# Kernel optimization log

Measured on AMD Instinct MI355X. Metric: run time of the kernel, lower is better.

## Reference

```python
import jax, jax.numpy as jnp
import numpy as np

EPS = 1e-5  # torch LayerNorm default

def _std(x):
    # standardize over the last 3 (tensor-feature) modes, biased variance like torch LayerNorm
    mu = jnp.mean(x, axis=(-3, -2, -1), keepdims=True)
    var = jnp.mean(jnp.square(x - mu), axis=(-3, -2, -1), keepdims=True)
    return (x - mu) * jax.lax.rsqrt(var + EPS)

def setup_inputs() -> dict:
    key = jax.random.key(0)
    ks = jax.random.split(key, 12)
    T, B = 512, 16
    a = b = c = 16          # input tensor modes (4096 features)
    ha = hb = hc = 8        # hidden tensor modes (512 features)
    G = 3                   # gates: r, z, n
    f32 = jnp.float32
    return {
        "x": jax.random.normal(ks[0], (T, B, a, b, c), f32),
        "h0": jnp.zeros((B, ha, hb, hc), f32),
        # input-to-hidden TCL3D factors + rank-1 bias + LN affines (stacked over 3 gates)
        "W_fa": jax.random.normal(ks[1], (G, a, ha), f32),
        "W_fb": jax.random.normal(ks[2], (G, b, hb), f32),
        "W_fc": jax.random.normal(ks[3], (G, c, hc), f32),
        "W_ba": jax.random.normal(ks[4], (G, ha), f32),
        "W_bb": jax.random.normal(ks[5], (G, hb), f32),
        "W_bc": jax.random.normal(ks[6], (G, hc), f32),
        "W_lnin_w": jnp.ones((G, a, b, c), f32),
        "W_lnin_b": jnp.zeros((G, a, b, c), f32),
        "W_lnout_w": jnp.ones((G, ha, hb, hc), f32),
        "W_lnout_b": jnp.zeros((G, ha, hb, hc), f32),
        # hidden-to-hidden TCL3D factors + rank-1 bias + LN affines
        "U_fa": jax.random.normal(ks[7], (G, ha, ha), f32),
        "U_fb": jax.random.normal(ks[8], (G, hb, hb), f32),
        "U_fc": jax.random.normal(ks[9], (G, hc, hc), f32),
        "U_ba": jax.random.normal(ks[10], (G, ha), f32),
        "U_bb": jax.random.normal(ks[11], (G, hb), f32),
        "U_bc": jax.random.normal(jax.random.fold_in(key, 99), (G, hc), f32),
        "U_lnin_w": jnp.ones((G, ha, hb, hc), f32),
        "U_lnin_b": jnp.zeros((G, ha, hb, hc), f32),
        "U_lnout_w": jnp.ones((G, ha, hb, hc), f32),
        "U_lnout_b": jnp.zeros((G, ha, hb, hc), f32),
    }

def reference(x, h0, W_fa, W_fb, W_fc, W_ba, W_bb, W_bc,
              W_lnin_w, W_lnin_b, W_lnout_w, W_lnout_b,
              U_fa, U_fb, U_fc, U_ba, U_bb, U_bc,
              U_lnin_w, U_lnin_b, U_lnout_w, U_lnout_b):
    # --- input-to-hidden TCL3D for all 3 gates, batched over time (no h dependence) ---
    xh = _std(x)                                                  # [T,B,a,b,c]
    xg = xh[None] * W_lnin_w[:, None, None] + W_lnin_b[:, None, None]  # [3,T,B,a,b,c]
    Wx = jnp.einsum('gtnabc,gad,gbe,gcf->gtndef', xg, W_fa, W_fb, W_fc)
    Wx = Wx + (W_ba[:, None, None, :, None, None]
               * W_bb[:, None, None, None, :, None]
               * W_bc[:, None, None, None, None, :])              # rank-1 bias
    Wx = _std(Wx) * W_lnout_w[:, None, None] + W_lnout_b[:, None, None]
    Wx = jnp.swapaxes(Wx, 0, 1)                                   # [T,3,B,ha,hb,hc]

    Ub = (U_ba[:, None, :, None, None]
          * U_bb[:, None, None, :, None]
          * U_bc[:, None, None, None, :])                         # [3,1,ha,hb,hc]

    def step(h, wx):
        # hidden-to-hidden TCL3D for all 3 gates
        hh = _std(h)                                              # [B,ha,hb,hc]
        hg = hh[None] * U_lnin_w[:, None] + U_lnin_b[:, None]     # [3,B,ha,hb,hc]
        Uh = jnp.einsum('gndef,gdp,geq,gfr->gnpqr', hg, U_fa, U_fb, U_fc) + Ub
        Uh = _std(Uh) * U_lnout_w[:, None] + U_lnout_b[:, None]
        r = jax.nn.sigmoid(wx[0] + Uh[0])
        z = jax.nn.sigmoid(wx[1] + Uh[1])
        n = jnp.tanh(wx[2] + r * Uh[2])
        h_new = (1.0 - z) * n + z * h
        return h_new, h_new

    _, outs = jax.lax.scan(step, h0, Wx)                          # [T,B,ha,hb,hc]
    return outs
```

## Files before the change

### kernel.cpp

```cpp
#include <hip/hip_runtime.h>

#define EPSV 1e-5f

#define KEEPV(x) asm volatile("" : "+v"(x))
#define KEEPS(x) asm volatile("" : "+s"(x))

#define DPP_XADD(v, ctrl)                                                  \
    v += __int_as_float(__builtin_amdgcn_update_dpp(                       \
        0, __float_as_int(v), ctrl, 0xF, 0xF, false))

__device__ __forceinline__ float wave_allsum(float v) {
    DPP_XADD(v, 0x128);
    DPP_XADD(v, 0x124);
    DPP_XADD(v, 0x122);
    DPP_XADD(v, 0x121);
    DPP_XADD(v, 0x142);
    DPP_XADD(v, 0x143);
    return __int_as_float(__builtin_amdgcn_readlane(__float_as_int(v), 63));
}

__device__ __forceinline__ void bar_lds() {
    asm volatile("s_waitcnt lgkmcnt(0)\n\ts_barrier" ::: "memory");
}

__global__ __launch_bounds__(256) void wx_kernel(
    const float* __restrict__ x,
    const float* __restrict__ Wfa, const float* __restrict__ Wfb,
    const float* __restrict__ Wfc,
    const float* __restrict__ Wba, const float* __restrict__ Wbb,
    const float* __restrict__ Wbc,
    const float* __restrict__ lniw, const float* __restrict__ lnib,
    const float* __restrict__ lnow, const float* __restrict__ lnob,
    float* __restrict__ wxo)
{
    __shared__ float POOL[4096 + 3*2048];
    __shared__ float baS[24], bbS[24], bcS[24];
    __shared__ float red[48];

    float* Xs = POOL;
    float* S1 = POOL + 4096;
    float* S2 = POOL;

    const int tid  = threadIdx.x;
    const int wid  = tid >> 6, lane = tid & 63;
    const size_t tb = blockIdx.x;
    const float* xp = x + tb * 4096;

    float s = 0.f, s2 = 0.f;
    for (int i = tid; i < 1024; i += 256) {
        const float4 v4 = ((const float4*)xp)[i];
        ((float4*)Xs)[i] = v4;
        s  += v4.x + v4.y + v4.z + v4.w;
        s2 += v4.x*v4.x + v4.y*v4.y + v4.z*v4.z + v4.w*v4.w;
    }
    if (tid < 24) { baS[tid] = Wba[tid]; bbS[tid] = Wbb[tid]; bcS[tid] = Wbc[tid]; }

    #pragma unroll
    for (int off = 32; off > 0; off >>= 1) {
        s  += __shfl_down(s,  off);
        s2 += __shfl_down(s2, off);
    }
    if (lane == 0) { red[wid] = s; red[8 + wid] = s2; }
    __syncthreads();
    s  = red[0] + red[1] + red[2] + red[3];
    s2 = red[8] + red[9] + red[10] + red[11];
    const float muX = s * (1.f / 4096.f);
    const float rsX = rsqrtf(fmaxf(s2 * (1.f / 4096.f) - muX * muX, 0.f) + EPSV);

    const int qh = __builtin_amdgcn_readfirstlane(tid >> 7);
    const int rh = __builtin_amdgcn_readfirstlane(tid >> 6);

    {
        float acc[3][8];
        #pragma unroll
        for (int g = 0; g < 3; ++g)
            #pragma unroll
            for (int p = 0; p < 8; ++p) acc[g][p] = 0.f;
        const int rest = tid;
        #pragma unroll
        for (int m = 0; m < 16; ++m) {
            const float xn = (Xs[m*256 + rest] - muX) * rsX;
            #pragma unroll
            for (int g = 0; g < 3; ++g) {
                const float xv = fmaf(xn, lniw[g*4096 + m*256 + rest],
                                      lnib[g*4096 + m*256 + rest]);
                #pragma unroll
                for (int p = 0; p < 8; ++p)
                    acc[g][p] = fmaf(xv, Wfa[(g*16 + m)*8 + p], acc[g][p]);
            }
        }
        #pragma unroll
        for (int g = 0; g < 3; ++g)
            #pragma unroll
            for (int p = 0; p < 8; ++p)
                S1[g*2048 + p*256 + (rest ^ (p << 3))] = acc[g][p];
    }
    __syncthreads();

    {
        float acc[3][4];
        #pragma unroll
        for (int g = 0; g < 3; ++g)
            #pragma unroll
            for (int j = 0; j < 4; ++j) acc[g][j] = 0.f;
        const int rest2 = tid & 127;
        const int c2 = rest2 >> 3, p2 = rest2 & 7;
        #pragma unroll
        for (int m = 0; m < 16; ++m) {
            const int off1 = p2*256 + (((m << 4) | c2) ^ (p2 << 3));
            #pragma unroll
            for (int g = 0; g < 3; ++g) {
                const float xv = S1[g*2048 + off1];
                #pragma unroll
                for (int j = 0; j < 4; ++j)
                    acc[g][j] = fmaf(xv, Wfb[(g*16 + m)*8 + qh*4 + j], acc[g][j]);
            }
        }
        #pragma unroll
        for (int g = 0; g < 3; ++g)
            #pragma unroll
            for (int j = 0; j < 4; ++j) {
                const int q = qh*4 + j;
                S2[g*1024 + q*128 + (rest2 ^ (q << 3))] = acc[g][j];
            }
    }
    __syncthreads();

    float v0[3], v1[3]; int idx0;
    {
        const int rest3 = tid & 63;
        const int q3 = rest3 & 7, pp = rest3 >> 3;
        float acc[3][2];
        #pragma unroll
        for (int g = 0; g < 3; ++g) { acc[g][0] = 0.f; acc[g][1] = 0.f; }
        #pragma unroll
        for (int m = 0; m < 16; ++m) {
            const int off2 = q3*128 + (((m << 3) | pp) ^ (q3 << 3));
            #pragma unroll
            for (int g = 0; g < 3; ++g) {
                const float xv = S2[g*1024 + off2];
                #pragma unroll
                for (int j = 0; j < 2; ++j)
                    acc[g][j] = fmaf(xv, Wfc[(g*16 + m)*8 + rh*2 + j], acc[g][j]);
            }
        }
        #pragma unroll
        for (int g = 0; g < 3; ++g) {
            const float bpq = baS[g*8 + pp] * bbS[g*8 + q3];
            v0[g] = acc[g][0] + bpq * bcS[g*8 + rh*2 + 0];
            v1[g] = acc[g][1] + bpq * bcS[g*8 + rh*2 + 1];
        }
        idx0 = rest3 * 8 + rh * 2;
    }

    {
        float t[3], t2[3];
        #pragma unroll
        for (int g = 0; g < 3; ++g) {
            t[g]  = v0[g] + v1[g];
            t2[g] = v0[g]*v0[g] + v1[g]*v1[g];
        }
        #pragma unroll
        for (int off = 32; off > 0; off >>= 1)
            #pragma unroll
            for (int g = 0; g < 3; ++g) {
                t[g]  += __shfl_down(t[g],  off);
                t2[g] += __shfl_down(t2[g], off);
            }
        if (lane == 0)
            #pragma unroll
            for (int g = 0; g < 3; ++g) {
                red[(g*2 + 0)*8 + wid] = t[g];
                red[(g*2 + 1)*8 + wid] = t2[g];
            }
        __syncthreads();
        #pragma unroll
        for (int g = 0; g < 3; ++g) {
            const float ts  = red[(g*2+0)*8+0] + red[(g*2+0)*8+1]
                            + red[(g*2+0)*8+2] + red[(g*2+0)*8+3];
            const float t2s = red[(g*2+1)*8+0] + red[(g*2+1)*8+1]
                            + red[(g*2+1)*8+2] + red[(g*2+1)*8+3];
            const float mu  = ts * (1.f / 512.f);
            const float var = fmaxf(t2s * (1.f / 512.f) - mu * mu, 0.f);
            const float rs  = rsqrtf(var + EPSV);
            float* wp = wxo + (tb * 3 + g) * 512;
            const float2 lw2 = *(const float2*)(lnow + g*512 + idx0);
            const float2 lb2 = *(const float2*)(lnob + g*512 + idx0);
            float2 o2;
            o2.x = fmaf((v0[g] - mu) * rs, lw2.x, lb2.x);
            o2.y = fmaf((v1[g] - mu) * rs, lw2.y, lb2.y);
            *(float2*)(wp + idx0) = o2;
        }
    }
}

__global__ __launch_bounds__(192)
__attribute__((amdgpu_waves_per_eu(1, 1)))
void scan_kernel(
    const float* __restrict__ wx,
    const float* __restrict__ h0,
    const float* __restrict__ Ufa, const float* __restrict__ Ufb,
    const float* __restrict__ Ufc,
    const float* __restrict__ Uba, const float* __restrict__ Ubb,
    const float* __restrict__ Ubc,
    const float* __restrict__ lniw, const float* __restrict__ lnib,
    const float* __restrict__ lnow, const float* __restrict__ lnob,
    float* __restrict__ out,
    int T, int B)
{
    const int n    = blockIdx.x;
    const int tid  = threadIdx.x;
    const int lane = tid & 63;
    const int gu   = __builtin_amdgcn_readfirstlane(tid >> 6);

    __shared__ float hgS[3][576];
    __shared__ float T1S[3][576];
    __shared__ float T2S[3][576];
    __shared__ float UhS[2][3][576];

    float wA[64], wB[64], wC[64];
    #pragma unroll
    for (int i = 0; i < 64; ++i) {
        wA[i] = __uint_as_float(__builtin_amdgcn_readfirstlane(
                    __float_as_uint(Ufa[gu*64 + i])));
        KEEPS(wA[i]);
    }
    #pragma unroll
    for (int i = 0; i < 64; ++i) { wB[i] = Ufb[gu*64 + i]; KEEPV(wB[i]); }
    #pragma unroll
    for (int i = 0; i < 64; ++i) { wC[i] = Ufc[gu*64 + i]; KEEPV(wC[i]); }

    float lnwT[8], lnbT[8], low8[8], lob8[8], ubias[8];
    {
        const int p_ = lane >> 3, q_ = lane & 7;
        const float bpq = Uba[gu*8 + p_] * Ubb[gu*8 + q_];
        #pragma unroll
        for (int k = 0; k < 8; ++k) {
            lnwT[k]  = lniw[gu*512 + k*64 + lane];
            lnbT[k]  = lnib[gu*512 + k*64 + lane];
            low8[k]  = lnow[gu*512 + lane*8 + k];
            lob8[k]  = lnob[gu*512 + lane*8 + k];
            ubias[k] = bpq * Ubc[gu*8 + k];
        }
    }

    const int wbase = lane;
    const int rbase = (lane & 7) * 72 + (lane >> 3);

    float hv[8];
    {
        const float4 a = *(const float4*)(h0 + n*512 + lane*8);
        const float4 b = *(const float4*)(h0 + n*512 + lane*8 + 4);
        hv[0]=a.x; hv[1]=a.y; hv[2]=a.z; hv[3]=a.w;
        hv[4]=b.x; hv[5]=b.y; hv[6]=b.z; hv[7]=b.w;
    }

    float uo[8];
    float pf[3][8];

#define LOADWX(TT)                                                         \
    {                                                                      \
        const float* base_ = wx + (((size_t)(TT) * B + n) * 3) * 512       \
                             + lane * 8;                                   \
        _Pragma("unroll")                                                  \
        for (int gg = 0; gg < 3; ++gg) {                                   \
            const float4 A_ = *(const float4*)(base_ + gg*512);            \
            const float4 B_ = *(const float4*)(base_ + gg*512 + 4);        \
            pf[gg][0]=A_.x; pf[gg][1]=A_.y; pf[gg][2]=A_.z; pf[gg][3]=A_.w;\
            pf[gg][4]=B_.x; pf[gg][5]=B_.y; pf[gg][6]=B_.z; pf[gg][7]=B_.w;\
        }                                                                  \
    }

#define WR8(BUFROW, V)                                                     \
    {                                                                      \
        float* p0_ = (BUFROW) + wbase;                                     \
        float* p1_ = p0_ + 288;                                            \
        p0_[0] = V[0]; p0_[72] = V[1]; p0_[144] = V[2]; p0_[216] = V[3];   \
        p1_[0] = V[4]; p1_[72] = V[5]; p1_[144] = V[6]; p1_[216] = V[7];   \
    }

#define RD8(BUFROW, V)                                                     \
    {                                                                      \
        const float* q_ = (BUFROW) + rbase;                                \
        V[0] = q_[0];  V[1] = q_[8];  V[2] = q_[16]; V[3] = q_[24];        \
        V[4] = q_[32]; V[5] = q_[40]; V[6] = q_[48]; V[7] = q_[56];        \
    }

#define RD8W(BUFROW, V)                                                    \
    {                                                                      \
        const float* q0_ = (BUFROW) + wbase;                               \
        const float* q1_ = q0_ + 288;                                      \
        V[0] = q0_[0]; V[1] = q0_[72]; V[2] = q0_[144]; V[3] = q0_[216];   \
        V[4] = q1_[0]; V[5] = q1_[72]; V[6] = q1_[144]; V[7] = q1_[216];   \
    }

#define PIPELINE(PARN)                                                     \
    {                                                                      \
        float xv_[8];                                                      \
        RD8(hgS[gu], xv_)                                                  \
        float sA = 0.f, sB = 0.f;                                          \
        _Pragma("unroll")                                                  \
        for (int k = 0; k < 8; ++k) { sA += hv[k]; sB += hv[k]*hv[k]; }    \
        sA = wave_allsum(sA); sB = wave_allsum(sB);                        \
        const float mu_ = sA * (1.f/512.f);                                \
        const float rs_ = rsqrtf(fmaxf(sB*(1.f/512.f) - mu_*mu_, 0.f)      \
                                 + EPSV);                                  \
        float a_[8];                                                       \
        _Pragma("unroll") for (int k = 0; k < 8; ++k) a_[k] = 0.f;         \
        _Pragma("unroll")                                                  \
        for (int m = 0; m < 8; ++m) {                                      \
            const float hgv = fmaf((xv_[m]-mu_)*rs_, lnwT[m], lnbT[m]);    \
            _Pragma("unroll")                                              \
            for (int q = 0; q < 8; ++q)                                    \
                a_[q] = fmaf(hgv, wA[m*8 + q], a_[q]);                     \
        }                                                                  \
        WR8(T1S[gu], a_)                                                   \
        RD8(T1S[gu], xv_)                                                  \
        _Pragma("unroll") for (int k = 0; k < 8; ++k) a_[k] = 0.f;         \
        _Pragma("unroll")                                                  \
        for (int m = 0; m < 8; ++m) {                                      \
            _Pragma("unroll")                                              \
            for (int q = 0; q < 8; ++q)                                    \
                a_[q] = fmaf(xv_[m], wB[m*8 + q], a_[q]);                  \
        }                                                                  \
        WR8(T2S[gu], a_)                                                   \
        RD8(T2S[gu], xv_)                                                  \
        _Pragma("unroll") for (int k = 0; k < 8; ++k) a_[k] = 0.f;         \
        _Pragma("unroll")                                                  \
        for (int m = 0; m < 8; ++m) {                                      \
            _Pragma("unroll")                                              \
            for (int q = 0; q < 8; ++q)                                    \
                a_[q] = fmaf(xv_[m], wC[m*8 + q], a_[q]);                  \
        }                                                                  \
        float sC = 0.f, sD = 0.f;                                          \
        _Pragma("unroll")                                                  \
        for (int k = 0; k < 8; ++k) {                                      \
            a_[k] += ubias[k]; sC += a_[k]; sD += a_[k]*a_[k];             \
        }                                                                  \
        sC = wave_allsum(sC); sD = wave_allsum(sD);                        \
        const float mu2_ = sC * (1.f/512.f);                               \
        const float rs2_ = rsqrtf(fmaxf(sD*(1.f/512.f) - mu2_*mu2_, 0.f)   \
                                  + EPSV);                                 \
        _Pragma("unroll")                                                  \
        for (int k = 0; k < 8; ++k)                                        \
            uo[k] = fmaf((a_[k]-mu2_)*rs2_, low8[k], lob8[k]);             \
        WR8(UhS[PARN][gu], uo)                                             \
    }

#define COMBINE(PARC, TT)                                                  \
    {                                                                      \
        float ur[8], uz[8], un[8];                                         \
        if (gu == 0) {                                                     \
            _Pragma("unroll")                                              \
            for (int k = 0; k < 8; ++k) ur[k] = uo[k];                     \
            RD8W(UhS[PARC][1], uz)                                         \
            RD8W(UhS[PARC][2], un)                                         \
        } else if (gu == 1) {                                              \
            _Pragma("unroll")                                              \
            for (int k = 0; k < 8; ++k) uz[k] = uo[k];                     \
            RD8W(UhS[PARC][0], ur)                                         \
            RD8W(UhS[PARC][2], un)                                         \
        } else {                                                           \
            _Pragma("unroll")                                              \
            for (int k = 0; k < 8; ++k) un[k] = uo[k];                     \
            RD8W(UhS[PARC][0], ur)                                         \
            RD8W(UhS[PARC][1], uz)                                         \
        }                                                                  \
        _Pragma("unroll")                                                  \
        for (int k = 0; k < 8; ++k) {                                      \
            const float er_ = __expf(-(pf[0][k] + ur[k]));                 \
            const float r_  = __builtin_amdgcn_rcpf(1.f + er_);            \
            const float ez_ = __expf(-(pf[1][k] + uz[k]));                 \
            const float z_  = __builtin_amdgcn_rcpf(1.f + ez_);            \
            const float e2_ = __expf(2.f * (pf[2][k] + r_ * un[k]));       \
            const float nn_ = 1.f - 2.f*__builtin_amdgcn_rcpf(e2_ + 1.f);  \
            hv[k] = (1.f - z_)*nn_ + z_*hv[k];                             \
        }                                                                  \
        WR8(hgS[gu], hv)      \
        if (gu == 0) {                                                     \
            float* op_ = out + ((size_t)(TT) * B + n) * 512 + lane*8;      \
            *(float4*)op_     = make_float4(hv[0], hv[1], hv[2], hv[3]);   \
            *(float4*)(op_+4) = make_float4(hv[4], hv[5], hv[6], hv[7]);   \
        }                                                                  \
    }

    LOADWX(0);
    WR8(hgS[gu], hv)
    PIPELINE(0);

    for (int t = 0; t < T; t += 2) {
        bar_lds();
        COMBINE(0, t)
        if (t + 1 < T) {
            LOADWX(t + 1);
            PIPELINE(1)
        }
        bar_lds();
        if (t + 1 < T) COMBINE(1, t + 1)
        if (t + 2 < T) {
            LOADWX(t + 2);
            PIPELINE(0)
        }
    }
#undef LOADWX
#undef WR8
#undef RD8
#undef RD8W
#undef PIPELINE
#undef COMBINE
}

extern "C" void kernel_launch(void* const* d_in, const int* in_sizes, int n_in,
                              void* d_out, int out_size, void* d_ws, size_t ws_size,
                              hipStream_t stream)
{
    const float* x    = (const float*)d_in[0];
    const float* h0   = (const float*)d_in[1];
    const float* Wfa  = (const float*)d_in[2];
    const float* Wfb  = (const float*)d_in[3];
    const float* Wfc  = (const float*)d_in[4];
    const float* Wba  = (const float*)d_in[5];
    const float* Wbb  = (const float*)d_in[6];
    const float* Wbc  = (const float*)d_in[7];
    const float* Wliw = (const float*)d_in[8];
    const float* Wlib = (const float*)d_in[9];
    const float* Wlow = (const float*)d_in[10];
    const float* Wlob = (const float*)d_in[11];
    const float* Ufa  = (const float*)d_in[12];
    const float* Ufb  = (const float*)d_in[13];
    const float* Ufc  = (const float*)d_in[14];
    const float* Uba  = (const float*)d_in[15];
    const float* Ubb  = (const float*)d_in[16];
    const float* Ubc  = (const float*)d_in[17];
    const float* Uliw = (const float*)d_in[18];
    const float* Ulib = (const float*)d_in[19];
    const float* Ulow = (const float*)d_in[20];
    const float* Ulob = (const float*)d_in[21];

    const int B = in_sizes[1] / 512;
    const int T = in_sizes[0] / (B * 4096);

    float* wxws = (float*)d_ws;
    float* out  = (float*)d_out;

    wx_kernel<<<T * B, 256, 0, stream>>>(x, Wfa, Wfb, Wfc, Wba, Wbb, Wbc,
                                         Wliw, Wlib, Wlow, Wlob, wxws);
    scan_kernel<<<B, 192, 0, stream>>>(wxws, h0, Ufa, Ufb, Ufc, Uba, Ubb, Ubc,
                                       Uliw, Ulib, Ulow, Ulob, out, T, B);
}
```

Before: 797.7 us.

## Fuse input projection and recurrent scan into one persistent kernel with chunk flags

Merges the per-timestep input TCL kernel and the sequential scan kernel into one launch. B blocks run the recurrence while 240 worker blocks compute Wx chunks of 16 timesteps and signal completion through global atomic counters, which the scan blocks poll before loading each chunk. The aim is to overlap the parallel input projection with the latency-bound scan instead of running them back to back. The scan blocks now launch with 256 threads and an idle fourth wave that only matches barriers. The design relies on all blocks being co-resident to avoid deadlock. The fallback branch passes a fixed shift that may not match other shapes.

```diff
diff --git a/kernel.cpp b/kernel.cpp
--- a/kernel.cpp
+++ b/kernel.cpp
@@ -4,6 +4,8 @@
 
 #define KEEPV(x) asm volatile("" : "+v"(x))
 #define KEEPS(x) asm volatile("" : "+s"(x))
+
+__device__ unsigned g_cnt[64];
 
 #define DPP_XADD(v, ctrl)                                                  \
     v += __int_as_float(__builtin_amdgcn_update_dpp(                       \
@@ -23,200 +25,219 @@
     asm volatile("s_waitcnt lgkmcnt(0)\n\ts_barrier" ::: "memory");
 }
 
-__global__ __launch_bounds__(256) void wx_kernel(
+__global__ void init_flags() {
+    if (threadIdx.x < 64) g_cnt[threadIdx.x] = 0u;
+}
+
+__global__ __launch_bounds__(256)
+__attribute__((amdgpu_waves_per_eu(1, 1)))
+void fused_kernel(
     const float* __restrict__ x,
     const float* __restrict__ Wfa, const float* __restrict__ Wfb,
     const float* __restrict__ Wfc,
     const float* __restrict__ Wba, const float* __restrict__ Wbb,
     const float* __restrict__ Wbc,
-    const float* __restrict__ lniw, const float* __restrict__ lnib,
-    const float* __restrict__ lnow, const float* __restrict__ lnob,
-    float* __restrict__ wxo)
-{
-    __shared__ float POOL[4096 + 3*2048];
-    __shared__ float baS[24], bbS[24], bcS[24];
-    __shared__ float red[48];
-
-    float* Xs = POOL;
-    float* S1 = POOL + 4096;
-    float* S2 = POOL;
-
-    const int tid  = threadIdx.x;
-    const int wid  = tid >> 6, lane = tid & 63;
-    const size_t tb = blockIdx.x;
-    const float* xp = x + tb * 4096;
-
-    float s = 0.f, s2 = 0.f;
-    for (int i = tid; i < 1024; i += 256) {
-        const float4 v4 = ((const float4*)xp)[i];
-        ((float4*)Xs)[i] = v4;
-        s  += v4.x + v4.y + v4.z + v4.w;
-        s2 += v4.x*v4.x + v4.y*v4.y + v4.z*v4.z + v4.w*v4.w;
-    }
-    if (tid < 24) { baS[tid] = Wba[tid]; bbS[tid] = Wbb[tid]; bcS[tid] = Wbc[tid]; }
-
-    #pragma unroll
-    for (int off = 32; off > 0; off >>= 1) {
-        s  += __shfl_down(s,  off);
-        s2 += __shfl_down(s2, off);
-    }
-    if (lane == 0) { red[wid] = s; red[8 + wid] = s2; }
-    __syncthreads();
-    s  = red[0] + red[1] + red[2] + red[3];
-    s2 = red[8] + red[9] + red[10] + red[11];
-    const float muX = s * (1.f / 4096.f);
-    const float rsX = rsqrtf(fmaxf(s2 * (1.f / 4096.f) - muX * muX, 0.f) + EPSV);
-
-    const int qh = __builtin_amdgcn_readfirstlane(tid >> 7);
-    const int rh = __builtin_amdgcn_readfirstlane(tid >> 6);
-
-    {
-        float acc[3][8];
-        #pragma unroll
-        for (int g = 0; g < 3; ++g)
-            #pragma unroll
-            for (int p = 0; p < 8; ++p) acc[g][p] = 0.f;
-        const int rest = tid;
-        #pragma unroll
-        for (int m = 0; m < 16; ++m) {
-            const float xn = (Xs[m*256 + rest] - muX) * rsX;
-            #pragma unroll
-            for (int g = 0; g < 3; ++g) {
-                const float xv = fmaf(xn, lniw[g*4096 + m*256 + rest],
-                                      lnib[g*4096 + m*256 + rest]);
-                #pragma unroll
-                for (int p = 0; p < 8; ++p)
-                    acc[g][p] = fmaf(xv, Wfa[(g*16 + m)*8 + p], acc[g][p]);
-            }
-        }
-        #pragma unroll
-        for (int g = 0; g < 3; ++g)
-            #pragma unroll
-            for (int p = 0; p < 8; ++p)
-                S1[g*2048 + p*256 + (rest ^ (p << 3))] = acc[g][p];
-    }
-    __syncthreads();
-
-    {
-        float acc[3][4];
-        #pragma unroll
-        for (int g = 0; g < 3; ++g)
-            #pragma unroll
-            for (int j = 0; j < 4; ++j) acc[g][j] = 0.f;
-        const int rest2 = tid & 127;
-        const int c2 = rest2 >> 3, p2 = rest2 & 7;
-        #pragma unroll
-        for (int m = 0; m < 16; ++m) {
-            const int off1 = p2*256 + (((m << 4) | c2) ^ (p2 << 3));
-            #pragma unroll
-            for (int g = 0; g < 3; ++g) {
-                const float xv = S1[g*2048 + off1];
-                #pragma unroll
-                for (int j = 0; j < 4; ++j)
-                    acc[g][j] = fmaf(xv, Wfb[(g*16 + m)*8 + qh*4 + j], acc[g][j]);
-            }
-        }
-        #pragma unroll
-        for (int g = 0; g < 3; ++g)
-            #pragma unroll
-            for (int j = 0; j < 4; ++j) {
-                const int q = qh*4 + j;
-                S2[g*1024 + q*128 + (rest2 ^ (q << 3))] = acc[g][j];
-            }
-    }
-    __syncthreads();
-
-    float v0[3], v1[3]; int idx0;
-    {
-        const int rest3 = tid & 63;
-        const int q3 = rest3 & 7, pp = rest3 >> 3;
-        float acc[3][2];
-        #pragma unroll
-        for (int g = 0; g < 3; ++g) { acc[g][0] = 0.f; acc[g][1] = 0.f; }
-        #pragma unroll
-        for (int m = 0; m < 16; ++m) {
-            const int off2 = q3*128 + (((m << 3) | pp) ^ (q3 << 3));
-            #pragma unroll
-            for (int g = 0; g < 3; ++g) {
-                const float xv = S2[g*1024 + off2];
-                #pragma unroll
-                for (int j = 0; j < 2; ++j)
-                    acc[g][j] = fmaf(xv, Wfc[(g*16 + m)*8 + rh*2 + j], acc[g][j]);
-            }
-        }
-        #pragma unroll
-        for (int g = 0; g < 3; ++g) {
-            const float bpq = baS[g*8 + pp] * bbS[g*8 + q3];
-            v0[g] = acc[g][0] + bpq * bcS[g*8 + rh*2 + 0];
-            v1[g] = acc[g][1] + bpq * bcS[g*8 + rh*2 + 1];
-        }
-        idx0 = rest3 * 8 + rh * 2;
-    }
-
-    {
-        float t[3], t2[3];
-        #pragma unroll
-        for (int g = 0; g < 3; ++g) {
-            t[g]  = v0[g] + v1[g];
-            t2[g] = v0[g]*v0[g] + v1[g]*v1[g];
-        }
-        #pragma unroll
-        for (int off = 32; off > 0; off >>= 1)
-            #pragma unroll
-            for (int g = 0; g < 3; ++g) {
-                t[g]  += __shfl_down(t[g],  off);
-                t2[g] += __shfl_down(t2[g], off);
-            }
-        if (lane == 0)
-            #pragma unroll
-            for (int g = 0; g < 3; ++g) {
-                red[(g*2 + 0)*8 + wid] = t[g];
-                red[(g*2 + 1)*8 + wid] = t2[g];
-            }
-        __syncthreads();
-        #pragma unroll
-        for (int g = 0; g < 3; ++g) {
-            const float ts  = red[(g*2+0)*8+0] + red[(g*2+0)*8+1]
-                            + red[(g*2+0)*8+2] + red[(g*2+0)*8+3];
-            const float t2s = red[(g*2+1)*8+0] + red[(g*2+1)*8+1]
-                            + red[(g*2+1)*8+2] + red[(g*2+1)*8+3];
-            const float mu  = ts * (1.f / 512.f);
-            const float var = fmaxf(t2s * (1.f / 512.f) - mu * mu, 0.f);
-            const float rs  = rsqrtf(var + EPSV);
-            float* wp = wxo + (tb * 3 + g) * 512;
-            const float2 lw2 = *(const float2*)(lnow + g*512 + idx0);
-            const float2 lb2 = *(const float2*)(lnob + g*512 + idx0);
-            float2 o2;
-            o2.x = fmaf((v0[g] - mu) * rs, lw2.x, lb2.x);
-            o2.y = fmaf((v1[g] - mu) * rs, lw2.y, lb2.y);
-            *(float2*)(wp + idx0) = o2;
-        }
-    }
-}
-
-__global__ __launch_bounds__(192)
-__attribute__((amdgpu_waves_per_eu(1, 1)))
-void scan_kernel(
-    const float* __restrict__ wx,
+    const float* __restrict__ Wliw, const float* __restrict__ Wlib,
+    const float* __restrict__ Wlow, const float* __restrict__ Wlob,
+    float* __restrict__ wxo,
     const float* __restrict__ h0,
     const float* __restrict__ Ufa, const float* __restrict__ Ufb,
     const float* __restrict__ Ufc,
     const float* __restrict__ Uba, const float* __restrict__ Ubb,
     const float* __restrict__ Ubc,
-    const float* __restrict__ lniw, const float* __restrict__ lnib,
-    const float* __restrict__ lnow, const float* __restrict__ lnob,
-    float* __restrict__ out,
-    int T, int B)
+    const float* __restrict__ Uliw, const float* __restrict__ Ulib,
+    const float* __restrict__ Ulow, const float* __restrict__ Ulob,
+    float* __restrict__ out, int T, int B, int nWx, int cshift)
 {
-    const int n    = blockIdx.x;
+    __shared__ __align__(16) float smem[10368];
     const int tid  = threadIdx.x;
     const int lane = tid & 63;
-    const int gu   = __builtin_amdgcn_readfirstlane(tid >> 6);
-
-    __shared__ float hgS[3][576];
-    __shared__ float T1S[3][576];
-    __shared__ float T2S[3][576];
-    __shared__ float UhS[2][3][576];
+
+    if ((int)blockIdx.x >= B) {
+        const int w  = blockIdx.x - B;
+        const int TB = T * B;
+        float* Xs  = smem;
+        float* S1  = smem + 4096;
+        float* S2  = smem;
+        float* baS = smem + 10240;
+        float* bbS = smem + 10264;
+        float* bcS = smem + 10288;
+        float* red = smem + 10312;
+
+        if (tid < 24) { baS[tid] = Wba[tid]; bbS[tid] = Wbb[tid]; bcS[tid] = Wbc[tid]; }
+        const int wid = tid >> 6;
+        const int qh = __builtin_amdgcn_readfirstlane(tid >> 7);
+        const int rh = __builtin_amdgcn_readfirstlane(tid >> 6);
+
+        for (int tb = w; tb < TB; tb += nWx) {
+            const float* xp = x + (size_t)tb * 4096;
+            float s = 0.f, s2 = 0.f;
+            for (int i = tid; i < 1024; i += 256) {
+                const float4 v4 = ((const float4*)xp)[i];
+                ((float4*)Xs)[i] = v4;
+                s  += v4.x + v4.y + v4.z + v4.w;
+                s2 += v4.x*v4.x + v4.y*v4.y + v4.z*v4.z + v4.w*v4.w;
+            }
+            #pragma unroll
+            for (int off = 32; off > 0; off >>= 1) {
+                s  += __shfl_down(s,  off);
+                s2 += __shfl_down(s2, off);
+            }
+            if (lane == 0) { red[wid] = s; red[8 + wid] = s2; }
+            __syncthreads();
+            s  = red[0] + red[1] + red[2] + red[3];
+            s2 = red[8] + red[9] + red[10] + red[11];
+            const float muX = s * (1.f / 4096.f);
+            const float rsX = rsqrtf(fmaxf(s2 * (1.f / 4096.f) - muX*muX, 0.f) + EPSV);
+
+            {
+                float acc[3][8];
+                #pragma unroll
+                for (int g = 0; g < 3; ++g)
+                    #pragma unroll
+                    for (int p = 0; p < 8; ++p) acc[g][p] = 0.f;
+                const int rest = tid;
+                #pragma unroll
+                for (int m = 0; m < 16; ++m) {
+                    const float xn = (Xs[m*256 + rest] - muX) * rsX;
+                    #pragma unroll
+                    for (int g = 0; g < 3; ++g) {
+                        const float xv = fmaf(xn, Wliw[g*4096 + m*256 + rest],
+                                              Wlib[g*4096 + m*256 + rest]);
+                        #pragma unroll
+                        for (int p = 0; p < 8; ++p)
+                            acc[g][p] = fmaf(xv, Wfa[(g*16 + m)*8 + p], acc[g][p]);
+                    }
+                }
+                #pragma unroll
+                for (int g = 0; g < 3; ++g)
+                    #pragma unroll
+                    for (int p = 0; p < 8; ++p)
+                        S1[g*2048 + p*256 + (rest ^ (p << 3))] = acc[g][p];
+            }
+            __syncthreads();
+
+            {
+                float acc[3][4];
+                #pragma unroll
+                for (int g = 0; g < 3; ++g)
+                    #pragma unroll
+                    for (int j = 0; j < 4; ++j) acc[g][j] = 0.f;
+                const int rest2 = tid & 127;
+                const int c2 = rest2 >> 3, p2 = rest2 & 7;
+                #pragma unroll
+                for (int m = 0; m < 16; ++m) {
+                    const int off1 = p2*256 + (((m << 4) | c2) ^ (p2 << 3));
+                    #pragma unroll
+                    for (int g = 0; g < 3; ++g) {
+                        const float xv = S1[g*2048 + off1];
+                        #pragma unroll
+                        for (int j = 0; j < 4; ++j)
+                            acc[g][j] = fmaf(xv, Wfb[(g*16 + m)*8 + qh*4 + j], acc[g][j]);
+                    }
+                }
+                #pragma unroll
+                for (int g = 0; g < 3; ++g)
+                    #pragma unroll
+                    for (int j = 0; j < 4; ++j) {
+                        const int q = qh*4 + j;
+                        S2[g*1024 + q*128 + (rest2 ^ (q << 3))] = acc[g][j];
+                    }
+            }
+            __syncthreads();
+
+            float v0[3], v1[3]; int idx0;
+            {
+                const int rest3 = tid & 63;
+                const int q3 = rest3 & 7, pp = rest3 >> 3;
+                float acc[3][2];
+                #pragma unroll
+                for (int g = 0; g < 3; ++g) { acc[g][0] = 0.f; acc[g][1] = 0.f; }
+                #pragma unroll
+                for (int m = 0; m < 16; ++m) {
+                    const int off2 = q3*128 + (((m << 3) | pp) ^ (q3 << 3));
+                    #pragma unroll
+                    for (int g = 0; g < 3; ++g) {
+                        const float xv = S2[g*1024 + off2];
+                        #pragma unroll
+                        for (int j = 0; j < 2; ++j)
+                            acc[g][j] = fmaf(xv, Wfc[(g*16 + m)*8 + rh*2 + j], acc[g][j]);
+                    }
+                }
+                #pragma unroll
+                for (int g = 0; g < 3; ++g) {
+                    const float bpq = baS[g*8 + pp] * bbS[g*8 + q3];
+                    v0[g] = acc[g][0] + bpq * bcS[g*8 + rh*2 + 0];
+                    v1[g] = acc[g][1] + bpq * bcS[g*8 + rh*2 + 1];
+                }
+                idx0 = rest3 * 8 + rh * 2;
+            }
+
+            {
+                float t[3], t2[3];
+                #pragma unroll
+                for (int g = 0; g < 3; ++g) {
+                    t[g]  = v0[g] + v1[g];
+                    t2[g] = v0[g]*v0[g] + v1[g]*v1[g];
+                }
+                #pragma unroll
+                for (int off = 32; off > 0; off >>= 1)
+                    #pragma unroll
+                    for (int g = 0; g < 3; ++g) {
+                        t[g]  += __shfl_down(t[g],  off);
+                        t2[g] += __shfl_down(t2[g], off);
+                    }
+                if (lane == 0)
+                    #pragma unroll
+                    for (int g = 0; g < 3; ++g) {
+                        red[(g*2 + 0)*8 + wid] = t[g];
+                        red[(g*2 + 1)*8 + wid] = t2[g];
+                    }
+                __syncthreads();
+                #pragma unroll
+                for (int g = 0; g < 3; ++g) {
+                    const float ts  = red[(g*2+0)*8+0] + red[(g*2+0)*8+1]
+                                    + red[(g*2+0)*8+2] + red[(g*2+0)*8+3];
+                    const float t2s = red[(g*2+1)*8+0] + red[(g*2+1)*8+1]
+                                    + red[(g*2+1)*8+2] + red[(g*2+1)*8+3];
+                    const float mu  = ts * (1.f / 512.f);
+                    const float var = fmaxf(t2s * (1.f / 512.f) - mu*mu, 0.f);
+                    const float rs  = rsqrtf(var + EPSV);
+                    float* wp = wxo + ((size_t)tb * 3 + g) * 512;
+                    const float2 lw2 = *(const float2*)(Wlow + g*512 + idx0);
+                    const float2 lb2 = *(const float2*)(Wlob + g*512 + idx0);
+                    float2 o2;
+                    o2.x = fmaf((v0[g] - mu) * rs, lw2.x, lb2.x);
+                    o2.y = fmaf((v1[g] - mu) * rs, lw2.y, lb2.y);
+                    *(float2*)(wp + idx0) = o2;
+                }
+            }
+            __threadfence();
+            __syncthreads();
+            if (tid == 0) atomicAdd(&g_cnt[tb >> cshift], 1u);
+        }
+        return;
+    }
+
+    const int n  = blockIdx.x;
+    const int gu = __builtin_amdgcn_readfirstlane(tid >> 6);
+
+    if (gu == 3) {
+        for (int t = 0; t < T; t += 2) { bar_lds(); bar_lds(); }
+        return;
+    }
+
+    float* hgS = smem;
+    float* T1S = smem + 1728;
+    float* T2S = smem + 3456;
+    float* UhS = smem + 5184;
+
+    const unsigned tgt_ = (unsigned)(B << 4);
+
+#define WAITCHUNK(C)                                                       \
+    while (__hip_atomic_load(&g_cnt[(C)], __ATOMIC_ACQUIRE,                \
+                             __HIP_MEMORY_SCOPE_AGENT) < tgt_)             \
+        __builtin_amdgcn_s_sleep(8);
 
     float wA[64], wB[64], wC[64];
     #pragma unroll
@@ -236,10 +257,10 @@
         const float bpq = Uba[gu*8 + p_] * Ubb[gu*8 + q_];
         #pragma unroll
         for (int k = 0; k < 8; ++k) {
-            lnwT[k]  = lniw[gu*512 + k*64 + lane];
-            lnbT[k]  = lnib[gu*512 + k*64 + lane];
-            low8[k]  = lnow[gu*512 + lane*8 + k];
-            lob8[k]  = lnob[gu*512 + lane*8 + k];
+            lnwT[k]  = Uliw[gu*512 + k*64 + lane];
+            lnbT[k]  = Ulib[gu*512 + k*64 + lane];
+            low8[k]  = Ulow[gu*512 + lane*8 + k];
+            lob8[k]  = Ulob[gu*512 + lane*8 + k];
             ubias[k] = bpq * Ubc[gu*8 + k];
         }
     }
@@ -260,7 +281,7 @@
 
 #define LOADWX(TT)                                                         \
     {                                                                      \
-        const float* base_ = wx + (((size_t)(TT) * B + n) * 3) * 512       \
+        const float* base_ = wxo + (((size_t)(TT) * B + n) * 3) * 512      \
                              + lane * 8;                                   \
         _Pragma("unroll")                                                  \
         for (int gg = 0; gg < 3; ++gg) {                                   \
@@ -297,7 +318,7 @@
 #define PIPELINE(PARN)                                                     \
     {                                                                      \
         float xv_[8];                                                      \
-        RD8(hgS[gu], xv_)                                                  \
+        RD8(hgS + gu*576, xv_)                                             \
         float sA = 0.f, sB = 0.f;                                          \
         _Pragma("unroll")                                                  \
         for (int k = 0; k < 8; ++k) { sA += hv[k]; sB += hv[k]*hv[k]; }    \
@@ -314,8 +335,8 @@
             for (int q = 0; q < 8; ++q)                                    \
                 a_[q] = fmaf(hgv, wA[m*8 + q], a_[q]);                     \
         }                                                                  \
-        WR8(T1S[gu], a_)                                                   \
-        RD8(T1S[gu], xv_)                                                  \
+        WR8(T1S + gu*576, a_)                                              \
+        RD8(T1S + gu*576, xv_)                                             \
         _Pragma("unroll") for (int k = 0; k < 8; ++k) a_[k] = 0.f;         \
         _Pragma("unroll")                                                  \
         for (int m = 0; m < 8; ++m) {                                      \
@@ -323,8 +344,8 @@
             for (int q = 0; q < 8; ++q)                                    \
                 a_[q] = fmaf(xv_[m], wB[m*8 + q], a_[q]);                  \
         }                                                                  \
-        WR8(T2S[gu], a_)                                                   \
-        RD8(T2S[gu], xv_)                                                  \
+        WR8(T2S + gu*576, a_)                                              \
+        RD8(T2S + gu*576, xv_)                                             \
         _Pragma("unroll") for (int k = 0; k < 8; ++k) a_[k] = 0.f;         \
         _Pragma("unroll")                                                  \
         for (int m = 0; m < 8; ++m) {                                      \
@@ -344,7 +365,7 @@
         _Pragma("unroll")                                                  \
         for (int k = 0; k < 8; ++k)                                        \
             uo[k] = fmaf((a_[k]-mu2_)*rs2_, low8[k], lob8[k]);             \
-        WR8(UhS[PARN][gu], uo)                                             \
+        WR8(UhS + ((PARN)*3 + gu)*576, uo)                                 \
     }
 
 #define COMBINE(PARC, TT)                                                  \
@@ -353,18 +374,18 @@
         if (gu == 0) {                                                     \
             _Pragma("unroll")                                              \
             for (int k = 0; k < 8; ++k) ur[k] = uo[k];                     \
-            RD8W(UhS[PARC][1], uz)                                         \
-            RD8W(UhS[PARC][2], un)                                         \
+            RD8W(UhS + ((PARC)*3 + 1)*576, uz)                             \
+            RD8W(UhS + ((PARC)*3 + 2)*576, un)                             \
         } else if (gu == 1) {                                              \
             _Pragma("unroll")                                              \
             for (int k = 0; k < 8; ++k) uz[k] = uo[k];                     \
-            RD8W(UhS[PARC][0], ur)                                         \
-            RD8W(UhS[PARC][2], un)                                         \
+            RD8W(UhS + ((PARC)*3 + 0)*576, ur)                             \
+            RD8W(UhS + ((PARC)*3 + 2)*576, un)                             \
         } else {                                                           \
             _Pragma("unroll")                                              \
             for (int k = 0; k < 8; ++k) un[k] = uo[k];                     \
-            RD8W(UhS[PARC][0], ur)                                         \
-            RD8W(UhS[PARC][1], uz)                                         \
+            RD8W(UhS + ((PARC)*3 + 0)*576, ur)                             \
+            RD8W(UhS + ((PARC)*3 + 1)*576, uz)                             \
         }                                                                  \
         _Pragma("unroll")                                                  \
         for (int k = 0; k < 8; ++k) {                                      \
@@ -376,7 +397,7 @@
             const float nn_ = 1.f - 2.f*__builtin_amdgcn_rcpf(e2_ + 1.f);  \
             hv[k] = (1.f - z_)*nn_ + z_*hv[k];                             \
         }                                                                  \
-        WR8(hgS[gu], hv)      \
+        WR8(hgS + gu*576, hv)                                              \
         if (gu == 0) {                                                     \
             float* op_ = out + ((size_t)(TT) * B + n) * 512 + lane*8;      \
             *(float4*)op_     = make_float4(hv[0], hv[1], hv[2], hv[3]);   \
@@ -384,8 +405,9 @@
         }                                                                  \
     }
 
+    WAITCHUNK(0)
     LOADWX(0);
-    WR8(hgS[gu], hv)
+    WR8(hgS + gu*576, hv)
     PIPELINE(0);
 
     for (int t = 0; t < T; t += 2) {
@@ -398,10 +420,12 @@
         bar_lds();
         if (t + 1 < T) COMBINE(1, t + 1)
         if (t + 2 < T) {
+            if (((t + 2) & 15) == 0) WAITCHUNK((t + 2) >> 4)
             LOADWX(t + 2);
             PIPELINE(0)
         }
     }
+#undef WAITCHUNK
 #undef LOADWX
 #undef WR8
 #undef RD8
@@ -443,8 +467,23 @@
     float* wxws = (float*)d_ws;
     float* out  = (float*)d_out;
 
-    wx_kernel<<<T * B, 256, 0, stream>>>(x, Wfa, Wfb, Wfc, Wba, Wbb, Wbc,
-                                         Wliw, Wlib, Wlow, Wlob, wxws);
-    scan_kernel<<<B, 192, 0, stream>>>(wxws, h0, Ufa, Ufb, Ufc, Uba, Ubb, Ubc,
-                                       Uliw, Ulib, Ulow, Ulob, out, T, B);
+    const int chunkTB = 16 * B;
+    const bool pow2   = (chunkTB & (chunkTB - 1)) == 0;
+    const int nWx     = 240;
+
+    if (pow2 && (T % 16 == 0) && (T / 16) <= 64 && B <= 16) {
+        int cshift = 0;
+        while ((1 << cshift) < chunkTB) ++cshift;
+        init_flags<<<1, 64, 0, stream>>>();
+        fused_kernel<<<B + nWx, 256, 0, stream>>>(
+            x, Wfa, Wfb, Wfc, Wba, Wbb, Wbc, Wliw, Wlib, Wlow, Wlob,
+            wxws, h0, Ufa, Ufb, Ufc, Uba, Ubb, Ubc, Uliw, Ulib, Ulow, Ulob,
+            out, T, B, nWx, cshift);
+    } else {
+        init_flags<<<1, 64, 0, stream>>>();
+        fused_kernel<<<B + nWx, 256, 0, stream>>>(
+            x, Wfa, Wfb, Wfc, Wba, Wbb, Wbc, Wliw, Wlib, Wlow, Wlob,
+            wxws, h0, Ufa, Ufb, Ufc, Uba, Ubb, Ubc, Uliw, Ulib, Ulow, Ulob,
+            out, T, B, nWx, 8);
+    }
 }
```

New measurement: 1.489 ms. +86.7%, slower.
